# Kernel optimization log

Hardware: AMD Instinct MI355X
Metric: run time of the kernel (lower is better)

The kernel has to match this reference:

```python
import jax, jax.numpy as jnp
import numpy as np

B, T, H = 4, 2048, 1024
NH = 16
DK = H // NH  # 64
EPS = 1e-12


def setup_inputs() -> dict:
    key = jax.random.key(0)
    ks = jax.random.split(key, 20)
    s = 0.02
    inp = {
        "hidden_states": jax.random.normal(ks[0], (B, T, H), jnp.float32),
        "source_states": jax.random.normal(ks[1], (B, T, H), jnp.float32),
        "source_len": jax.random.randint(ks[2], (B,), 0, T, jnp.int64),
        # attention params (Linear: y = x @ W + b)
        "Wq": s * jax.random.normal(ks[3], (H, H), jnp.float32),
        "bq": jnp.zeros((H,), jnp.float32),
        "Wk": s * jax.random.normal(ks[4], (H, H), jnp.float32),
        "bk": jnp.zeros((H,), jnp.float32),
        "Wv": s * jax.random.normal(ks[5], (H, H), jnp.float32),
        "bv": jnp.zeros((H,), jnp.float32),
        "Wd": s * jax.random.normal(ks[6], (H, H), jnp.float32),
        "bd": jnp.zeros((H,), jnp.float32),
        # Fp: Linear -> ReLU -> (dropout, eval=id) -> Linear -> (dropout)
        "Wp1": s * jax.random.normal(ks[7], (H, H), jnp.float32),
        "bp1": jnp.zeros((H,), jnp.float32),
        "Wp2": s * jax.random.normal(ks[8], (H, H), jnp.float32),
        "bp2": jnp.zeros((H,), jnp.float32),
        # LayerNorm
        "ln_g": jnp.ones((H,), jnp.float32),
        "ln_b": jnp.zeros((H,), jnp.float32),
    }
    return inp


def _split_heads(x):
    # (B, T, H) -> (B, NH, T, DK)
    return x.reshape(B, T, NH, DK).transpose(0, 2, 1, 3)


def reference(hidden_states, source_states, source_len, Wq, bq, Wk, bk, Wv, bv,
              Wd, bd, Wp1, bp1, Wp2, bp2, ln_g, ln_b):
    # P = Fp(source_states), masked to valid source positions
    P = jax.nn.relu(source_states @ Wp1 + bp1) @ Wp2 + bp2  # (B,T,H)
    rng = jnp.arange(T)[None, :]                              # (1,T)
    source_mask = rng < source_len[:, None]                   # (B,T) bool
    P = P * source_mask[:, :, None].astype(P.dtype)

    q = _split_heads(hidden_states @ Wq + bq)  # (B,NH,T,DK)
    k = _split_heads(P @ Wk + bk)
    v = _split_heads(P @ Wv + bv)

    scores = jnp.einsum('bhqd,bhkd->bhqk', q, k) / jnp.sqrt(jnp.float32(DK))
    scores = scores + (1.0 - source_mask[:, None, None, :].astype(scores.dtype)) * -10000.0
    probs = jax.nn.softmax(scores.astype(jnp.float32), axis=-1).astype(hidden_states.dtype)

    ctx = jnp.einsum('bhqk,bhkd->bhqd', probs, v)            # (B,NH,T,DK)
    ctx = ctx.transpose(0, 2, 1, 3).reshape(B, T, H)

    attn_out = ctx @ Wd + bd
    x = attn_out + hidden_states
    mu = jnp.mean(x, axis=-1, keepdims=True)
    var = jnp.mean(jnp.square(x - mu), axis=-1, keepdims=True)
    out = (x - mu) * jax.lax.rsqrt(var + EPS) * ln_g + ln_b
    return out
```

## Files before the change

kernel.cpp:

```cpp
#include <hip/hip_runtime.h>
#include <hip/hip_bf16.h>

#define BB 4
#define TT 2048
#define HH 1024
#define NHH 16
#define DKK 64

typedef __attribute__((ext_vector_type(8))) short bf16x8;
typedef __attribute__((ext_vector_type(4))) float f32x4;

__device__ __forceinline__ unsigned short f2bf(float f) {
    union { float f; unsigned u; } v; v.f = f;
    unsigned r = v.u + 0x7fffu + ((v.u >> 16) & 1u);
    return (unsigned short)(r >> 16);
}

__device__ __forceinline__ void gload_lds16(const unsigned short* g, unsigned short* l) {
    __builtin_amdgcn_global_load_lds(
        (const __attribute__((address_space(1))) unsigned int*)g,
        (__attribute__((address_space(3))) unsigned int*)l, 16, 0, 0);
}

__global__ __launch_bounds__(256) void cvt_kernel(const float* __restrict__ in,
                                                  unsigned short* __restrict__ out, int n4) {
    int i = blockIdx.x * blockDim.x + threadIdx.x;
    if (i < n4) {
        float4 v = reinterpret_cast<const float4*>(in)[i];
        union { unsigned short u[4]; unsigned long long ll; } o;
        o.u[0] = f2bf(v.x); o.u[1] = f2bf(v.y); o.u[2] = f2bf(v.z); o.u[3] = f2bf(v.w);
        reinterpret_cast<unsigned long long*>(out)[i] = o.ll;
    }
}

__global__ __launch_bounds__(256) void wtcvt_kernel(const float* __restrict__ W,
                                                    unsigned short* __restrict__ Wt) {
    __shared__ float t[32][33];
    int bx = blockIdx.x * 32, by = blockIdx.y * 32;
    int tx = threadIdx.x, ty = threadIdx.y;
#pragma unroll
    for (int i = 0; i < 32; i += 8)
        t[ty + i][tx] = W[(size_t)(by + ty + i) * HH + bx + tx];
    __syncthreads();
#pragma unroll
    for (int i = 0; i < 32; i += 8)
        Wt[(size_t)(bx + ty + i) * HH + by + tx] = f2bf(t[tx][ty + i]);
}

template <int EPI, bool SKIP>
__global__ __launch_bounds__(256) void gemm_kernel(
    const unsigned short* __restrict__ A, const unsigned short* __restrict__ Bt,
    const float* __restrict__ bias, unsigned short* __restrict__ Cb,
    float* __restrict__ Cf, const float* __restrict__ resid,
    const int* __restrict__ slen, int M, int N, int K) {
    __shared__ unsigned short As[128 * 64];
    __shared__ unsigned short Bs[128 * 64];
    int by = blockIdx.y * 128, bx = blockIdx.x * 128;
    if constexpr (SKIP) {
        int slb = slen[by >> 11];
        int ktend = ((slb + 63) >> 6) << 6;
        if (ktend == 0) ktend = 64;
        if ((by & (TT - 1)) >= ktend) return;
    }
    int tid = threadIdx.x, lane = tid & 63, w = tid >> 6;
    int wr = (w >> 1) * 64, wc = (w & 1) * 64;

    f32x4 acc[4][4] = {};
    for (int k0 = 0; k0 < K; k0 += 64) {
        __syncthreads();
#pragma unroll
        for (int c = 0; c < 4; c++) {
            int idx = c * 256 + tid;
            int r = idx >> 3, col = (idx & 7) * 8;
            gload_lds16(&A[(size_t)(by + r) * K + k0 + col], &As[idx * 8]);
            gload_lds16(&Bt[(size_t)(bx + r) * K + k0 + col], &Bs[idx * 8]);
        }
        __syncthreads();
#pragma unroll
        for (int kk = 0; kk < 2; kk++) {
            bf16x8 a[4], b[4];
#pragma unroll
            for (int i = 0; i < 4; i++)
                a[i] = *(bf16x8*)&As[(wr + i * 16 + (lane & 15)) * 64 + kk * 32 + (lane >> 4) * 8];
#pragma unroll
            for (int j = 0; j < 4; j++)
                b[j] = *(bf16x8*)&Bs[(wc + j * 16 + (lane & 15)) * 64 + kk * 32 + (lane >> 4) * 8];
#pragma unroll
            for (int i = 0; i < 4; i++)
#pragma unroll
                for (int j = 0; j < 4; j++)
                    acc[i][j] = __builtin_amdgcn_mfma_f32_16x16x32_bf16(a[i], b[j], acc[i][j], 0, 0, 0);
        }
    }

    int sl = 0;
    if constexpr (EPI == 2) sl = slen[by >> 11];
#pragma unroll
    for (int i = 0; i < 4; i++)
#pragma unroll
        for (int j = 0; j < 4; j++)
#pragma unroll
            for (int r = 0; r < 4; r++) {
                int row = by + wr + i * 16 + (lane >> 4) * 4 + r;
                int col = bx + wc + j * 16 + (lane & 15);
                float v = acc[i][j][r] + bias[col];
                if constexpr (EPI == 1) v = fmaxf(v, 0.f);
                if constexpr (EPI == 2) { int t = row & (TT - 1); if (t >= sl) v = 0.f; }
                if constexpr (EPI == 6) v *= 0.18033688f;
                if constexpr (EPI == 1 || EPI == 2) {
                    Cb[(size_t)row * N + col] = f2bf(v);
                } else if constexpr (EPI == 3 || EPI == 6) {
                    int b = row >> 11, t = row & (TT - 1), h = col >> 6, d = col & 63;
                    Cb[((size_t)((b * NHH + h) * TT + t)) * DKK + d] = f2bf(v);
                } else if constexpr (EPI == 4) {
                    int b = row >> 11, t = row & (TT - 1), h = col >> 6, d = col & 63;
                    Cb[((size_t)((b * NHH + h) * DKK + d)) * TT + t] = f2bf(v);
                } else if constexpr (EPI == 5) {
                    Cf[(size_t)row * N + col] = v + resid[(size_t)row * N + col];
                }
            }
}

__global__ __launch_bounds__(512) void attn_kernel(
    const unsigned short* __restrict__ Q, const unsigned short* __restrict__ K,
    const unsigned short* __restrict__ Vt, const int* __restrict__ slen,
    unsigned short* __restrict__ ctx) {
    __shared__ unsigned short Ks[64 * 64];
    __shared__ unsigned short Vs[64 * 64];
    __shared__ unsigned short Pl[8][16 * 64];
    int tid = threadIdx.x, lane = tid & 63, w = tid >> 6;
    int c = lane & 15, g = lane >> 4;
    int b = blockIdx.z, h = blockIdx.y, q0 = blockIdx.x * 128;
    size_t bh = (size_t)(b * NHH + h);
    int sl = slen[b];
    int ktend = ((sl + 63) >> 6) << 6;
    if (ktend == 0) ktend = 64;

    bf16x8 qf[2];
    int qrow = q0 + w * 16 + c;
#pragma unroll
    for (int half = 0; half < 2; half++)
        qf[half] = *(const bf16x8*)&Q[(bh * TT + qrow) * DKK + half * 32 + g * 8];

    char* Pw = (char*)&Pl[w][0];
    unsigned swz = (unsigned)((c & 7) << 4);

    int sr = tid >> 3, ss = tid & 7;
    int scol = (ss ^ (sr & 7)) * 8;

    float m_ = -INFINITY, l_ = 0.f;
    f32x4 o[4] = {};

    for (int kt = 0; kt < ktend; kt += 64) {
        __syncthreads();
        gload_lds16(&K[(bh * TT + kt + sr) * DKK + scol], &Ks[tid * 8]);
        gload_lds16(&Vt[(bh * DKK + sr) * TT + kt + scol], &Vs[tid * 8]);
        __syncthreads();

        f32x4 s[4] = {};
        __builtin_amdgcn_s_setprio(1);
#pragma unroll
        for (int j = 0; j < 4; j++)
#pragma unroll
            for (int half = 0; half < 2; half++) {
                bf16x8 kf = *(bf16x8*)((char*)Ks + (j * 16 + c) * 128 +
                                       (((unsigned)(half * 64 + g * 16)) ^ swz));
                s[j] = __builtin_amdgcn_mfma_f32_16x16x32_bf16(kf, qf[half], s[j], 0, 0, 0);
            }
        __builtin_amdgcn_s_setprio(0);

        if (kt + 64 > sl) {
#pragma unroll
            for (int j = 0; j < 4; j++) {
                int kbase = kt + j * 16 + g * 4;
#pragma unroll
                for (int r = 0; r < 4; r++)
                    if (kbase + r >= sl) s[j][r] = -14427.0f;
            }
        }

        float tmax = -INFINITY;
#pragma unroll
        for (int j = 0; j < 4; j++)
#pragma unroll
            for (int r = 0; r < 4; r++) tmax = fmaxf(tmax, s[j][r]);
        tmax = fmaxf(tmax, __shfl_xor(tmax, 16));
        tmax = fmaxf(tmax, __shfl_xor(tmax, 32));

        float p[4][4];
        float ps = 0.f;
        if (__all(tmax <= m_ + 8.f)) {
#pragma unroll
            for (int j = 0; j < 4; j++)
#pragma unroll
                for (int r = 0; r < 4; r++) {
                    p[j][r] = __builtin_amdgcn_exp2f(s[j][r] - m_);
                    ps += p[j][r];
                }
            ps += __shfl_xor(ps, 16);
            ps += __shfl_xor(ps, 32);
            l_ += ps;
        } else {
            float mn = fmaxf(m_, tmax);
            float alpha = __builtin_amdgcn_exp2f(m_ - mn);
#pragma unroll
            for (int j = 0; j < 4; j++)
#pragma unroll
                for (int r = 0; r < 4; r++) {
                    p[j][r] = __builtin_amdgcn_exp2f(s[j][r] - mn);
                    ps += p[j][r];
                }
            ps += __shfl_xor(ps, 16);
            ps += __shfl_xor(ps, 32);
            l_ = l_ * alpha + ps;
            m_ = mn;
            float av[4];
#pragma unroll
            for (int r = 0; r < 4; r++) av[r] = __shfl(alpha, g * 4 + r);
#pragma unroll
            for (int go = 0; go < 4; go++)
#pragma unroll
                for (int r = 0; r < 4; r++) o[go][r] *= av[r];
        }

#pragma unroll
        for (int j = 0; j < 4; j++) {
            __hip_bfloat162 lo = __float22bfloat162_rn(make_float2(p[j][0], p[j][1]));
            __hip_bfloat162 hi = __float22bfloat162_rn(make_float2(p[j][2], p[j][3]));
            uint2 u;
            u.x = *(unsigned*)&lo;
            u.y = *(unsigned*)&hi;
            *(uint2*)(Pw + c * 128 + (((unsigned)(j * 32 + g * 8)) ^ swz)) = u;
        }
        bf16x8 pf0 = *(bf16x8*)(Pw + c * 128 + (((unsigned)(g * 16)) ^ swz));
        bf16x8 pf1 = *(bf16x8*)(Pw + c * 128 + (((unsigned)(64 + g * 16)) ^ swz));

        __builtin_amdgcn_s_setprio(1);
#pragma unroll
        for (int go = 0; go < 4; go++) {
            bf16x8 vf0 = *(bf16x8*)((char*)Vs + (go * 16 + c) * 128 +
                                    (((unsigned)(g * 16)) ^ swz));
            o[go] = __builtin_amdgcn_mfma_f32_16x16x32_bf16(pf0, vf0, o[go], 0, 0, 0);
            bf16x8 vf1 = *(bf16x8*)((char*)Vs + (go * 16 + c) * 128 +
                                    (((unsigned)(64 + g * 16)) ^ swz));
            o[go] = __builtin_amdgcn_mfma_f32_16x16x32_bf16(pf1, vf1, o[go], 0, 0, 0);
        }
        __builtin_amdgcn_s_setprio(0);
    }

    float linv[4];
#pragma unroll
    for (int r = 0; r < 4; r++) linv[r] = 1.f / __shfl(l_, g * 4 + r);
#pragma unroll
    for (int go = 0; go < 4; go++)
#pragma unroll
        for (int r = 0; r < 4; r++) {
            int t = q0 + w * 16 + g * 4 + r;
            int col = h * DKK + go * 16 + c;
            ctx[((size_t)(b * TT + t)) * HH + col] = f2bf(o[go][r] * linv[r]);
        }
}

__global__ __launch_bounds__(256) void ln_kernel(float* __restrict__ x,
                                                 const float* __restrict__ gam,
                                                 const float* __restrict__ bet) {
    int row = blockIdx.x, tid = threadIdx.x;
    float4 v = reinterpret_cast<float4*>(x)[(size_t)row * 256 + tid];
    float s = v.x + v.y + v.z + v.w;
#pragma unroll
    for (int m = 1; m < 64; m <<= 1) s += __shfl_xor(s, m);
    __shared__ float red[4], red2[4];
    if ((tid & 63) == 0) red[tid >> 6] = s;
    __syncthreads();
    float mean = (red[0] + red[1] + red[2] + red[3]) * (1.f / 1024.f);
    float dx0 = v.x - mean, dx1 = v.y - mean, dx2 = v.z - mean, dx3 = v.w - mean;
    float ss = dx0 * dx0 + dx1 * dx1 + dx2 * dx2 + dx3 * dx3;
#pragma unroll
    for (int m = 1; m < 64; m <<= 1) ss += __shfl_xor(ss, m);
    if ((tid & 63) == 0) red2[tid >> 6] = ss;
    __syncthreads();
    float var = (red2[0] + red2[1] + red2[2] + red2[3]) * (1.f / 1024.f);
    float rs = rsqrtf(var + 1e-12f);
    int c = tid * 4;
    float4 ov;
    ov.x = dx0 * rs * gam[c + 0] + bet[c + 0];
    ov.y = dx1 * rs * gam[c + 1] + bet[c + 1];
    ov.z = dx2 * rs * gam[c + 2] + bet[c + 2];
    ov.w = dx3 * rs * gam[c + 3] + bet[c + 3];
    reinterpret_cast<float4*>(x)[(size_t)row * 256 + tid] = ov;
}

extern "C" void kernel_launch(void* const* d_in, const int* in_sizes, int n_in,
                              void* d_out, int out_size, void* d_ws, size_t ws_size,
                              hipStream_t stream) {
    const float* hid  = (const float*)d_in[0];
    const float* src  = (const float*)d_in[1];
    const int* slen   = (const int*)d_in[2];
    const float* Wq  = (const float*)d_in[3];  const float* bq  = (const float*)d_in[4];
    const float* Wk  = (const float*)d_in[5];  const float* bk  = (const float*)d_in[6];
    const float* Wv  = (const float*)d_in[7];  const float* bv  = (const float*)d_in[8];
    const float* Wd  = (const float*)d_in[9];  const float* bd  = (const float*)d_in[10];
    const float* Wp1 = (const float*)d_in[11]; const float* bp1 = (const float*)d_in[12];
    const float* Wp2 = (const float*)d_in[13]; const float* bp2 = (const float*)d_in[14];
    const float* lng = (const float*)d_in[15]; const float* lnb = (const float*)d_in[16];

    char* ws = (char*)d_ws;
    const size_t MB = 1ull << 20;
    unsigned short* Wqt  = (unsigned short*)(ws + 0 * MB);
    unsigned short* Wkt  = (unsigned short*)(ws + 2 * MB);
    unsigned short* Wvt  = (unsigned short*)(ws + 4 * MB);
    unsigned short* Wdt  = (unsigned short*)(ws + 6 * MB);
    unsigned short* Wp1t = (unsigned short*)(ws + 8 * MB);
    unsigned short* Wp2t = (unsigned short*)(ws + 10 * MB);
    unsigned short* hidb = (unsigned short*)(ws + 12 * MB);
    unsigned short* srcb = (unsigned short*)(ws + 28 * MB);
    unsigned short* Ptmp = (unsigned short*)(ws + 44 * MB);
    unsigned short* Pb   = (unsigned short*)(ws + 60 * MB);
    unsigned short* Qb   = (unsigned short*)(ws + 76 * MB);
    unsigned short* Kb   = hidb;
    unsigned short* Vtb  = Ptmp;
    unsigned short* ctxb = srcb;

    dim3 tb(32, 8);
    wtcvt_kernel<<<dim3(32, 32), tb, 0, stream>>>(Wq, Wqt);
    wtcvt_kernel<<<dim3(32, 32), tb, 0, stream>>>(Wk, Wkt);
    wtcvt_kernel<<<dim3(32, 32), tb, 0, stream>>>(Wv, Wvt);
    wtcvt_kernel<<<dim3(32, 32), tb, 0, stream>>>(Wd, Wdt);
    wtcvt_kernel<<<dim3(32, 32), tb, 0, stream>>>(Wp1, Wp1t);
    wtcvt_kernel<<<dim3(32, 32), tb, 0, stream>>>(Wp2, Wp2t);

    const int n4 = (BB * TT * HH) / 4;
    cvt_kernel<<<n4 / 256, 256, 0, stream>>>(hid, hidb, n4);
    cvt_kernel<<<n4 / 256, 256, 0, stream>>>(src, srcb, n4);

    dim3 gg(HH / 128, (BB * TT) / 128);
    gemm_kernel<1, true><<<gg, 256, 0, stream>>>(srcb, Wp1t, bp1, Ptmp, nullptr, nullptr, slen, BB * TT, HH, HH);
    gemm_kernel<2, true><<<gg, 256, 0, stream>>>(Ptmp, Wp2t, bp2, Pb, nullptr, nullptr, slen, BB * TT, HH, HH);
    gemm_kernel<6, false><<<gg, 256, 0, stream>>>(hidb, Wqt, bq, Qb, nullptr, nullptr, slen, BB * TT, HH, HH);
    gemm_kernel<3, true><<<gg, 256, 0, stream>>>(Pb, Wkt, bk, Kb, nullptr, nullptr, slen, BB * TT, HH, HH);
    gemm_kernel<4, true><<<gg, 256, 0, stream>>>(Pb, Wvt, bv, Vtb, nullptr, nullptr, slen, BB * TT, HH, HH);
    attn_kernel<<<dim3(TT / 128, NHH, BB), 512, 0, stream>>>(Qb, Kb, Vtb, slen, ctxb);
    gemm_kernel<5, false><<<gg, 256, 0, stream>>>(ctxb, Wdt, bd, nullptr, (float*)d_out, hid, slen, BB * TT, HH, HH);
    ln_kernel<<<BB * TT, 256, 0, stream>>>((float*)d_out, lng, lnb);
}
```

Measured before the change: 286.1 us.

## Merge QKV GEMMs, batch weight/input conversions, double-buffer attention K/V tiles

Merges the six weight transpose-convert launches into one kernel and the two input conversions into one, cutting launch overhead. The Q, K and V projections now run in a single grid with per-sector dispatch, which exposes more parallelism per launch; the skip of masked K/V rows is kept. The attention kernel double-buffers its K/V shared-memory tiles so the next tile's global loads are issued while the current tile is being computed. In exchange, shared memory use in attention grows, and the new QKV kernel uses an unswizzled LDS layout that may bank-conflict.

Result: faster. 272.7 us (-4.7%).

```diff
diff --git a/kernel.cpp b/kernel.cpp
--- a/kernel.cpp
+++ b/kernel.cpp
@@ -22,8 +22,12 @@
         (__attribute__((address_space(3))) unsigned int*)l, 16, 0, 0);
 }
 
-__global__ __launch_bounds__(256) void cvt_kernel(const float* __restrict__ in,
-                                                  unsigned short* __restrict__ out, int n4) {
+__global__ __launch_bounds__(256) void cvt2_kernel(const float* __restrict__ in0,
+                                                   const float* __restrict__ in1,
+                                                   unsigned short* __restrict__ out0,
+                                                   unsigned short* __restrict__ out1, int n4) {
+    const float* in = blockIdx.y ? in1 : in0;
+    unsigned short* out = blockIdx.y ? out1 : out0;
     int i = blockIdx.x * blockDim.x + threadIdx.x;
     if (i < n4) {
         float4 v = reinterpret_cast<const float4*>(in)[i];
@@ -33,8 +37,20 @@
     }
 }
 
-__global__ __launch_bounds__(256) void wtcvt_kernel(const float* __restrict__ W,
-                                                    unsigned short* __restrict__ Wt) {
+__global__ __launch_bounds__(256) void wtcvt6_kernel(
+    const float* __restrict__ W0, const float* __restrict__ W1, const float* __restrict__ W2,
+    const float* __restrict__ W3, const float* __restrict__ W4, const float* __restrict__ W5,
+    unsigned short* __restrict__ T0, unsigned short* __restrict__ T1, unsigned short* __restrict__ T2,
+    unsigned short* __restrict__ T3, unsigned short* __restrict__ T4, unsigned short* __restrict__ T5) {
+    const float* W; unsigned short* Wt;
+    switch (blockIdx.z) {
+        case 0: W = W0; Wt = T0; break;
+        case 1: W = W1; Wt = T1; break;
+        case 2: W = W2; Wt = T2; break;
+        case 3: W = W3; Wt = T3; break;
+        case 4: W = W4; Wt = T4; break;
+        default: W = W5; Wt = T5; break;
+    }
     __shared__ float t[32][33];
     int bx = blockIdx.x * 32, by = blockIdx.y * 32;
     int tx = threadIdx.x, ty = threadIdx.y;
@@ -106,27 +122,93 @@
                 float v = acc[i][j][r] + bias[col];
                 if constexpr (EPI == 1) v = fmaxf(v, 0.f);
                 if constexpr (EPI == 2) { int t = row & (TT - 1); if (t >= sl) v = 0.f; }
-                if constexpr (EPI == 6) v *= 0.18033688f;
                 if constexpr (EPI == 1 || EPI == 2) {
                     Cb[(size_t)row * N + col] = f2bf(v);
-                } else if constexpr (EPI == 3 || EPI == 6) {
-                    int b = row >> 11, t = row & (TT - 1), h = col >> 6, d = col & 63;
-                    Cb[((size_t)((b * NHH + h) * TT + t)) * DKK + d] = f2bf(v);
-                } else if constexpr (EPI == 4) {
-                    int b = row >> 11, t = row & (TT - 1), h = col >> 6, d = col & 63;
-                    Cb[((size_t)((b * NHH + h) * DKK + d)) * TT + t] = f2bf(v);
                 } else if constexpr (EPI == 5) {
                     Cf[(size_t)row * N + col] = v + resid[(size_t)row * N + col];
                 }
             }
 }
 
+__global__ __launch_bounds__(256) void qkv_gemm_kernel(
+    const unsigned short* __restrict__ hidb, const unsigned short* __restrict__ Pb,
+    const unsigned short* __restrict__ Wqt, const unsigned short* __restrict__ Wkt,
+    const unsigned short* __restrict__ Wvt,
+    const float* __restrict__ bq, const float* __restrict__ bk, const float* __restrict__ bv,
+    unsigned short* __restrict__ Qb, unsigned short* __restrict__ Kb,
+    unsigned short* __restrict__ Vtb, const int* __restrict__ slen) {
+    __shared__ unsigned short As[128 * 64];
+    __shared__ unsigned short Bs[128 * 64];
+    int sector = blockIdx.x >> 3;
+    int bx = (blockIdx.x & 7) * 128;
+    int by = blockIdx.y * 128;
+    int slb = slen[by >> 11];
+    int ktend = ((slb + 63) >> 6) << 6;
+    if (ktend == 0) ktend = 64;
+    if (sector != 0 && (by & (TT - 1)) >= ktend) return;
+
+    const unsigned short* A  = (sector == 0) ? hidb : Pb;
+    const unsigned short* Bt = (sector == 0) ? Wqt : ((sector == 1) ? Wkt : Wvt);
+    const float* bias        = (sector == 0) ? bq : ((sector == 1) ? bk : bv);
+
+    int tid = threadIdx.x, lane = tid & 63, w = tid >> 6;
+    int wr = (w >> 1) * 64, wc = (w & 1) * 64;
+
+    f32x4 acc[4][4] = {};
+    for (int k0 = 0; k0 < HH; k0 += 64) {
+        __syncthreads();
+#pragma unroll
+        for (int c = 0; c < 4; c++) {
+            int idx = c * 256 + tid;
+            int r = idx >> 3, col = (idx & 7) * 8;
+            gload_lds16(&A[(size_t)(by + r) * HH + k0 + col], &As[idx * 8]);
+            gload_lds16(&Bt[(size_t)(bx + r) * HH + k0 + col], &Bs[idx * 8]);
+        }
+        __syncthreads();
+#pragma unroll
+        for (int kk = 0; kk < 2; kk++) {
+            bf16x8 a[4], b[4];
+#pragma unroll
+            for (int i = 0; i < 4; i++)
+                a[i] = *(bf16x8*)&As[(wr + i * 16 + (lane & 15)) * 64 + kk * 32 + (lane >> 4) * 8];
+#pragma unroll
+            for (int j = 0; j < 4; j++)
+                b[j] = *(bf16x8*)&Bs[(wc + j * 16 + (lane & 15)) * 64 + kk * 32 + (lane >> 4) * 8];
+#pragma unroll
+            for (int i = 0; i < 4; i++)
+#pragma unroll
+                for (int j = 0; j < 4; j++)
+                    acc[i][j] = __builtin_amdgcn_mfma_f32_16x16x32_bf16(a[i], b[j], acc[i][j], 0, 0, 0);
+        }
+    }
+
+#pragma unroll
+    for (int i = 0; i < 4; i++)
+#pragma unroll
+        for (int j = 0; j < 4; j++)
+#pragma unroll
+            for (int r = 0; r < 4; r++) {
+                int row = by + wr + i * 16 + (lane >> 4) * 4 + r;
+                int col = bx + wc + j * 16 + (lane & 15);
+                float v = acc[i][j][r] + bias[col];
+                int b = row >> 11, t = row & (TT - 1), h = col >> 6, d = col & 63;
+                if (sector == 0) {
+                    v *= 0.18033688f;
+                    Qb[((size_t)((b * NHH + h) * TT + t)) * DKK + d] = f2bf(v);
+                } else if (sector == 1) {
+                    Kb[((size_t)((b * NHH + h) * TT + t)) * DKK + d] = f2bf(v);
+                } else {
+                    Vtb[((size_t)((b * NHH + h) * DKK + d)) * TT + t] = f2bf(v);
+                }
+            }
+}
+
 __global__ __launch_bounds__(512) void attn_kernel(
     const unsigned short* __restrict__ Q, const unsigned short* __restrict__ K,
     const unsigned short* __restrict__ Vt, const int* __restrict__ slen,
     unsigned short* __restrict__ ctx) {
-    __shared__ unsigned short Ks[64 * 64];
-    __shared__ unsigned short Vs[64 * 64];
+    __shared__ unsigned short Ks[2][64 * 64];
+    __shared__ unsigned short Vs[2][64 * 64];
     __shared__ unsigned short Pl[8][16 * 64];
     int tid = threadIdx.x, lane = tid & 63, w = tid >> 6;
     int c = lane & 15, g = lane >> 4;
@@ -148,14 +230,19 @@
     int sr = tid >> 3, ss = tid & 7;
     int scol = (ss ^ (sr & 7)) * 8;
 
+    gload_lds16(&K[(bh * TT + sr) * DKK + scol], &Ks[0][tid * 8]);
+    gload_lds16(&Vt[(bh * DKK + sr) * TT + scol], &Vs[0][tid * 8]);
+    int cur = 0;
+
     float m_ = -INFINITY, l_ = 0.f;
     f32x4 o[4] = {};
 
     for (int kt = 0; kt < ktend; kt += 64) {
         __syncthreads();
-        gload_lds16(&K[(bh * TT + kt + sr) * DKK + scol], &Ks[tid * 8]);
-        gload_lds16(&Vt[(bh * DKK + sr) * TT + kt + scol], &Vs[tid * 8]);
-        __syncthreads();
+        if (kt + 64 < ktend) {
+            gload_lds16(&K[(bh * TT + kt + 64 + sr) * DKK + scol], &Ks[cur ^ 1][tid * 8]);
+            gload_lds16(&Vt[(bh * DKK + sr) * TT + kt + 64 + scol], &Vs[cur ^ 1][tid * 8]);
+        }
 
         f32x4 s[4] = {};
         __builtin_amdgcn_s_setprio(1);
@@ -163,7 +250,7 @@
         for (int j = 0; j < 4; j++)
 #pragma unroll
             for (int half = 0; half < 2; half++) {
-                bf16x8 kf = *(bf16x8*)((char*)Ks + (j * 16 + c) * 128 +
+                bf16x8 kf = *(bf16x8*)((char*)&Ks[cur][0] + (j * 16 + c) * 128 +
                                        (((unsigned)(half * 64 + g * 16)) ^ swz));
                 s[j] = __builtin_amdgcn_mfma_f32_16x16x32_bf16(kf, qf[half], s[j], 0, 0, 0);
             }
@@ -238,14 +325,15 @@
         __builtin_amdgcn_s_setprio(1);
 #pragma unroll
         for (int go = 0; go < 4; go++) {
-            bf16x8 vf0 = *(bf16x8*)((char*)Vs + (go * 16 + c) * 128 +
+            bf16x8 vf0 = *(bf16x8*)((char*)&Vs[cur][0] + (go * 16 + c) * 128 +
                                     (((unsigned)(g * 16)) ^ swz));
             o[go] = __builtin_amdgcn_mfma_f32_16x16x32_bf16(pf0, vf0, o[go], 0, 0, 0);
-            bf16x8 vf1 = *(bf16x8*)((char*)Vs + (go * 16 + c) * 128 +
+            bf16x8 vf1 = *(bf16x8*)((char*)&Vs[cur][0] + (go * 16 + c) * 128 +
                                     (((unsigned)(64 + g * 16)) ^ swz));
             o[go] = __builtin_amdgcn_mfma_f32_16x16x32_bf16(pf1, vf1, o[go], 0, 0, 0);
         }
         __builtin_amdgcn_s_setprio(0);
+        cur ^= 1;
     }
 
     float linv[4];
@@ -321,24 +409,17 @@
     unsigned short* Vtb  = Ptmp;
     unsigned short* ctxb = srcb;
 
-    dim3 tb(32, 8);
-    wtcvt_kernel<<<dim3(32, 32), tb, 0, stream>>>(Wq, Wqt);
-    wtcvt_kernel<<<dim3(32, 32), tb, 0, stream>>>(Wk, Wkt);
-    wtcvt_kernel<<<dim3(32, 32), tb, 0, stream>>>(Wv, Wvt);
-    wtcvt_kernel<<<dim3(32, 32), tb, 0, stream>>>(Wd, Wdt);
-    wtcvt_kernel<<<dim3(32, 32), tb, 0, stream>>>(Wp1, Wp1t);
-    wtcvt_kernel<<<dim3(32, 32), tb, 0, stream>>>(Wp2, Wp2t);
+    wtcvt6_kernel<<<dim3(32, 32, 6), dim3(32, 8), 0, stream>>>(
+        Wq, Wk, Wv, Wd, Wp1, Wp2, Wqt, Wkt, Wvt, Wdt, Wp1t, Wp2t);
 
     const int n4 = (BB * TT * HH) / 4;
-    cvt_kernel<<<n4 / 256, 256, 0, stream>>>(hid, hidb, n4);
-    cvt_kernel<<<n4 / 256, 256, 0, stream>>>(src, srcb, n4);
+    cvt2_kernel<<<dim3(n4 / 256, 2), 256, 0, stream>>>(hid, src, hidb, srcb, n4);
 
     dim3 gg(HH / 128, (BB * TT) / 128);
     gemm_kernel<1, true><<<gg, 256, 0, stream>>>(srcb, Wp1t, bp1, Ptmp, nullptr, nullptr, slen, BB * TT, HH, HH);
     gemm_kernel<2, true><<<gg, 256, 0, stream>>>(Ptmp, Wp2t, bp2, Pb, nullptr, nullptr, slen, BB * TT, HH, HH);
-    gemm_kernel<6, false><<<gg, 256, 0, stream>>>(hidb, Wqt, bq, Qb, nullptr, nullptr, slen, BB * TT, HH, HH);
-    gemm_kernel<3, true><<<gg, 256, 0, stream>>>(Pb, Wkt, bk, Kb, nullptr, nullptr, slen, BB * TT, HH, HH);
-    gemm_kernel<4, true><<<gg, 256, 0, stream>>>(Pb, Wvt, bv, Vtb, nullptr, nullptr, slen, BB * TT, HH, HH);
+    qkv_gemm_kernel<<<dim3(24, 64), 256, 0, stream>>>(
+        hidb, Pb, Wqt, Wkt, Wvt, bq, bk, bv, Qb, Kb, Vtb, slen);
     attn_kernel<<<dim3(TT / 128, NHH, BB), 512, 0, stream>>>(Qb, Kb, Vtb, slen, ctxb);
     gemm_kernel<5, false><<<gg, 256, 0, stream>>>(ctxb, Wdt, bd, nullptr, (float*)d_out, hid, slen, BB * TT, HH, HH);
     ln_kernel<<<BB * TT, 256, 0, stream>>>((float*)d_out, lng, lnb);
```

## Double-buffer attention K/V tiles, remap GEMM blocks per XCD, batch conversion launches

Applied to the files above, without the earlier changes.

The attention kernel now keeps two LDS buffers for K and V. It prefetches the next 64-key tile while computing on the current one, which replaces the load-then-barrier stall on every iteration. The GEMM block index is remapped so consecutive flat block IDs, which are assigned round-robin across XCDs, group row tiles per XCD to improve L2 reuse. The six weight-transpose launches and two input-cast launches are merged into one launch each to cut launch overhead. The risk is that the compiler's vmcnt handling around global_load_lds may serialize the prefetch, and the extra LDS may lower occupancy.

New measurement: 269.5 us. 1.06x faster.

```diff
diff --git a/kernel.cpp b/kernel.cpp
--- a/kernel.cpp
+++ b/kernel.cpp
@@ -22,8 +22,12 @@
         (__attribute__((address_space(3))) unsigned int*)l, 16, 0, 0);
 }
 
-__global__ __launch_bounds__(256) void cvt_kernel(const float* __restrict__ in,
-                                                  unsigned short* __restrict__ out, int n4) {
+__global__ __launch_bounds__(256) void cvt2_kernel(const float* __restrict__ in0,
+                                                   const float* __restrict__ in1,
+                                                   unsigned short* __restrict__ out0,
+                                                   unsigned short* __restrict__ out1, int n4) {
+    const float* in = blockIdx.y ? in1 : in0;
+    unsigned short* out = blockIdx.y ? out1 : out0;
     int i = blockIdx.x * blockDim.x + threadIdx.x;
     if (i < n4) {
         float4 v = reinterpret_cast<const float4*>(in)[i];
@@ -33,8 +37,20 @@
     }
 }
 
-__global__ __launch_bounds__(256) void wtcvt_kernel(const float* __restrict__ W,
-                                                    unsigned short* __restrict__ Wt) {
+__global__ __launch_bounds__(256) void wtcvt6_kernel(
+    const float* __restrict__ W0, const float* __restrict__ W1, const float* __restrict__ W2,
+    const float* __restrict__ W3, const float* __restrict__ W4, const float* __restrict__ W5,
+    unsigned short* __restrict__ T0, unsigned short* __restrict__ T1, unsigned short* __restrict__ T2,
+    unsigned short* __restrict__ T3, unsigned short* __restrict__ T4, unsigned short* __restrict__ T5) {
+    const float* W; unsigned short* Wt;
+    switch (blockIdx.z) {
+        case 0: W = W0; Wt = T0; break;
+        case 1: W = W1; Wt = T1; break;
+        case 2: W = W2; Wt = T2; break;
+        case 3: W = W3; Wt = T3; break;
+        case 4: W = W4; Wt = T4; break;
+        default: W = W5; Wt = T5; break;
+    }
     __shared__ float t[32][33];
     int bx = blockIdx.x * 32, by = blockIdx.y * 32;
     int tx = threadIdx.x, ty = threadIdx.y;
@@ -55,7 +71,10 @@
     const int* __restrict__ slen, int M, int N, int K) {
     __shared__ unsigned short As[128 * 64];
     __shared__ unsigned short Bs[128 * 64];
-    int by = blockIdx.y * 128, bx = blockIdx.x * 128;
+    int flat = blockIdx.y * 8 + blockIdx.x;
+    int xcd = flat & 7, idx = flat >> 3;
+    int bx = (idx & 7) * 128;
+    int by = (xcd + ((idx >> 3) << 3)) * 128;
     if constexpr (SKIP) {
         int slb = slen[by >> 11];
         int ktend = ((slb + 63) >> 6) << 6;
@@ -70,10 +89,10 @@
         __syncthreads();
 #pragma unroll
         for (int c = 0; c < 4; c++) {
-            int idx = c * 256 + tid;
-            int r = idx >> 3, col = (idx & 7) * 8;
-            gload_lds16(&A[(size_t)(by + r) * K + k0 + col], &As[idx * 8]);
-            gload_lds16(&Bt[(size_t)(bx + r) * K + k0 + col], &Bs[idx * 8]);
+            int idx2 = c * 256 + tid;
+            int r = idx2 >> 3, col = (idx2 & 7) * 8;
+            gload_lds16(&A[(size_t)(by + r) * K + k0 + col], &As[idx2 * 8]);
+            gload_lds16(&Bt[(size_t)(bx + r) * K + k0 + col], &Bs[idx2 * 8]);
         }
         __syncthreads();
 #pragma unroll
@@ -125,8 +144,8 @@
     const unsigned short* __restrict__ Q, const unsigned short* __restrict__ K,
     const unsigned short* __restrict__ Vt, const int* __restrict__ slen,
     unsigned short* __restrict__ ctx) {
-    __shared__ unsigned short Ks[64 * 64];
-    __shared__ unsigned short Vs[64 * 64];
+    __shared__ unsigned short Ks[2][64 * 64];
+    __shared__ unsigned short Vs[2][64 * 64];
     __shared__ unsigned short Pl[8][16 * 64];
     int tid = threadIdx.x, lane = tid & 63, w = tid >> 6;
     int c = lane & 15, g = lane >> 4;
@@ -148,14 +167,19 @@
     int sr = tid >> 3, ss = tid & 7;
     int scol = (ss ^ (sr & 7)) * 8;
 
+    gload_lds16(&K[(bh * TT + sr) * DKK + scol], &Ks[0][tid * 8]);
+    gload_lds16(&Vt[(bh * DKK + sr) * TT + scol], &Vs[0][tid * 8]);
+    int cur = 0;
+
     float m_ = -INFINITY, l_ = 0.f;
     f32x4 o[4] = {};
 
     for (int kt = 0; kt < ktend; kt += 64) {
         __syncthreads();
-        gload_lds16(&K[(bh * TT + kt + sr) * DKK + scol], &Ks[tid * 8]);
-        gload_lds16(&Vt[(bh * DKK + sr) * TT + kt + scol], &Vs[tid * 8]);
-        __syncthreads();
+        if (kt + 64 < ktend) {
+            gload_lds16(&K[(bh * TT + kt + 64 + sr) * DKK + scol], &Ks[cur ^ 1][tid * 8]);
+            gload_lds16(&Vt[(bh * DKK + sr) * TT + kt + 64 + scol], &Vs[cur ^ 1][tid * 8]);
+        }
 
         f32x4 s[4] = {};
         __builtin_amdgcn_s_setprio(1);
@@ -163,7 +187,7 @@
         for (int j = 0; j < 4; j++)
 #pragma unroll
             for (int half = 0; half < 2; half++) {
-                bf16x8 kf = *(bf16x8*)((char*)Ks + (j * 16 + c) * 128 +
+                bf16x8 kf = *(bf16x8*)((char*)&Ks[cur][0] + (j * 16 + c) * 128 +
                                        (((unsigned)(half * 64 + g * 16)) ^ swz));
                 s[j] = __builtin_amdgcn_mfma_f32_16x16x32_bf16(kf, qf[half], s[j], 0, 0, 0);
             }
@@ -238,14 +262,15 @@
         __builtin_amdgcn_s_setprio(1);
 #pragma unroll
         for (int go = 0; go < 4; go++) {
-            bf16x8 vf0 = *(bf16x8*)((char*)Vs + (go * 16 + c) * 128 +
+            bf16x8 vf0 = *(bf16x8*)((char*)&Vs[cur][0] + (go * 16 + c) * 128 +
                                     (((unsigned)(g * 16)) ^ swz));
             o[go] = __builtin_amdgcn_mfma_f32_16x16x32_bf16(pf0, vf0, o[go], 0, 0, 0);
-            bf16x8 vf1 = *(bf16x8*)((char*)Vs + (go * 16 + c) * 128 +
+            bf16x8 vf1 = *(bf16x8*)((char*)&Vs[cur][0] + (go * 16 + c) * 128 +
                                     (((unsigned)(64 + g * 16)) ^ swz));
             o[go] = __builtin_amdgcn_mfma_f32_16x16x32_bf16(pf1, vf1, o[go], 0, 0, 0);
         }
         __builtin_amdgcn_s_setprio(0);
+        cur ^= 1;
     }
 
     float linv[4];
@@ -321,19 +346,13 @@
     unsigned short* Vtb  = Ptmp;
     unsigned short* ctxb = srcb;
 
-    dim3 tb(32, 8);
-    wtcvt_kernel<<<dim3(32, 32), tb, 0, stream>>>(Wq, Wqt);
-    wtcvt_kernel<<<dim3(32, 32), tb, 0, stream>>>(Wk, Wkt);
-    wtcvt_kernel<<<dim3(32, 32), tb, 0, stream>>>(Wv, Wvt);
-    wtcvt_kernel<<<dim3(32, 32), tb, 0, stream>>>(Wd, Wdt);
-    wtcvt_kernel<<<dim3(32, 32), tb, 0, stream>>>(Wp1, Wp1t);
-    wtcvt_kernel<<<dim3(32, 32), tb, 0, stream>>>(Wp2, Wp2t);
+    wtcvt6_kernel<<<dim3(32, 32, 6), dim3(32, 8), 0, stream>>>(
+        Wq, Wk, Wv, Wd, Wp1, Wp2, Wqt, Wkt, Wvt, Wdt, Wp1t, Wp2t);
 
     const int n4 = (BB * TT * HH) / 4;
-    cvt_kernel<<<n4 / 256, 256, 0, stream>>>(hid, hidb, n4);
-    cvt_kernel<<<n4 / 256, 256, 0, stream>>>(src, srcb, n4);
-
-    dim3 gg(HH / 128, (BB * TT) / 128);
+    cvt2_kernel<<<dim3(n4 / 256, 2), 256, 0, stream>>>(hid, src, hidb, srcb, n4);
+
+    dim3 gg(8, 64);
     gemm_kernel<1, true><<<gg, 256, 0, stream>>>(srcb, Wp1t, bp1, Ptmp, nullptr, nullptr, slen, BB * TT, HH, HH);
     gemm_kernel<2, true><<<gg, 256, 0, stream>>>(Ptmp, Wp2t, bp2, Pb, nullptr, nullptr, slen, BB * TT, HH, HH);
     gemm_kernel<6, false><<<gg, 256, 0, stream>>>(hidb, Wqt, bq, Qb, nullptr, nullptr, slen, BB * TT, HH, HH);
```
